# Kernel optimization log

Hardware: AMD Instinct MI355X
Metric: run time of the kernel (lower is better)

## Reference

```python
import jax, jax.numpy as jnp
import numpy as np

B, L, LF = 4096, 200, 100
E, P, H = 64, 32, 32      # embed_dim, prompt_embed_dim, prompt_net_hidden_size
IV, UV = 100000, 50000    # item/user vocab
IFD, UFD = 128, 128       # item/user raw feature dims
PNET = E * H + H + H * P + P  # per-sample MLP param count


def _forward(item_emb, user_emb, W_if, b_if, W_uf, b_uf, Wp, bp,
             Wf1, bf1, Wf2, bf2, Wf3, item_features, user_features,
             user_id, target_item_id, history_item_id, history_len,
             item_pos_feedback, item_pos_feedback_mask,
             item_neg_feedback, item_neg_feedback_mask):
    # ---- backbone embeddings ----
    tgt = item_emb[target_item_id]              # [B,E]
    hist = item_emb[history_item_id]            # [B,L,E]
    item_feat_e = jax.nn.sigmoid(item_features @ W_if + b_if)   # [B,E]
    user_feat_e = jax.nn.sigmoid(user_features @ W_uf + b_uf)   # [B,E]
    # attention sequence pooling over history (length-masked softmax)
    valid = jnp.arange(L)[None, :] < history_len[:, None]        # [B,L]
    scores = jnp.einsum('be,ble->bl', tgt, hist) / jnp.sqrt(jnp.float32(E))
    scores = jnp.where(valid, scores, jnp.float32(-1e9))
    attn = jax.nn.softmax(scores, axis=-1)
    hist_pooled = jnp.einsum('bl,ble->be', attn, hist)           # [B,E]
    final_user_embed = user_emb[user_id] + user_feat_e + hist_pooled  # [B,E]
    final_item_embed = tgt + item_feat_e                              # [B,E]

    # ---- prompt input: masked mean over positive feedback ----
    pos_fb = item_emb[item_pos_feedback]        # [B,LF,E]
    pm = item_pos_feedback_mask.astype(jnp.float32)   # [B,LF,1]
    prompt_input = (pos_fb * pm).sum(axis=1) / pm.sum(axis=1)   # [B,E]

    # ---- hypernetwork: generate per-sample MLP weights ----
    total_prompt = jax.nn.relu(prompt_input @ Wp + bp)  # [B, P+PNET]
    prompt_embed = total_prompt[:, :P]
    pnet = total_prompt[:, P:]
    s1 = E * H
    w1 = pnet[:, :s1].reshape(-1, E, H)                 # [B,E,H]
    b1 = pnet[:, s1:s1 + H]                             # [B,H]
    w2 = pnet[:, s1 + H:s1 + H + H * P].reshape(-1, H, P)  # [B,H,P]
    b2 = pnet[:, s1 + H + H * P:]                       # [B,P]

    def prompt_mlp(u):  # u: [B,Lf,E] -> [B,Lf,P]
        h = jax.nn.relu(jnp.einsum('ble,beh->blh', u, w1) + b1[:, None, :])
        return jnp.einsum('blh,bhp->blp', h, w2) + b2[:, None, :]

    pos_pe = jnp.where(item_pos_feedback_mask, prompt_mlp(pos_fb), 0.0).sum(axis=1)  # [B,P]
    neg_fb = item_emb[item_neg_feedback]
    neg_pe = jnp.where(item_neg_feedback_mask, prompt_mlp(neg_fb), 0.0).sum(axis=1)  # [B,P]
    loss_pfpe = jax.nn.softplus(-(pos_pe - neg_pe))     # [B,P]

    # ---- fusion + dot-product scoring ----
    fusion_in = jnp.concatenate([final_item_embed, pos_pe, prompt_embed], axis=1)  # [B,E+2P]
    h = jax.nn.relu(fusion_in @ Wf1 + bf1)
    h = jax.nn.relu(h @ Wf2 + bf2)
    fused_item = h @ Wf3                                # [B,E], last layer: no bias/act
    output = jnp.sum(final_user_embed * fused_item, axis=1, keepdims=True)  # [B,1]
    return output, loss_pfpe


def setup_inputs() -> dict:
    key = jax.random.key(0)
    ks = jax.random.split(key, 20)
    g = lambda i, shape, s=0.05: jax.random.normal(ks[i], shape, jnp.float32) * s
    pm = jax.random.randint(ks[14], (B, LF, 1), 0, 2).astype(bool).at[:, 0, :].set(True)
    nm = jax.random.randint(ks[15], (B, LF, 1), 0, 2).astype(bool).at[:, 0, :].set(True)
    return {
        'item_emb': g(0, (IV, E)),
        'user_emb': g(1, (UV, E)),
        'W_if': g(2, (IFD, E)), 'b_if': jnp.zeros((E,), jnp.float32),
        'W_uf': g(3, (UFD, E)), 'b_uf': jnp.zeros((E,), jnp.float32),
        'Wp': g(4, (E, P + PNET)), 'bp': jnp.zeros((P + PNET,), jnp.float32),
        'Wf1': g(5, (E + 2 * P, 200)), 'bf1': jnp.zeros((200,), jnp.float32),
        'Wf2': g(6, (200, 80)), 'bf2': jnp.zeros((80,), jnp.float32),
        'Wf3': g(7, (80, E)),
        'item_features': jax.random.normal(ks[8], (B, IFD), jnp.float32),
        'user_features': jax.random.normal(ks[9], (B, UFD), jnp.float32),
        'user_id': jax.random.randint(ks[10], (B,), 0, UV),
        'target_item_id': jax.random.randint(ks[11], (B,), 0, IV),
        'history_item_id': jax.random.randint(ks[12], (B, L), 0, IV),
        'history_len': jax.random.randint(ks[13], (B,), 1, L + 1),
        'item_pos_feedback': jax.random.randint(ks[16], (B, LF), 0, IV),
        'item_pos_feedback_mask': pm,
        'item_neg_feedback': jax.random.randint(ks[17], (B, LF), 0, IV),
        'item_neg_feedback_mask': nm,
    }


def reference(item_emb, user_emb, W_if, b_if, W_uf, b_uf, Wp, bp,
              Wf1, bf1, Wf2, bf2, Wf3, item_features, user_features,
              user_id, target_item_id, history_item_id, history_len,
              item_pos_feedback, item_pos_feedback_mask,
              item_neg_feedback, item_neg_feedback_mask):
    return _forward(item_emb, user_emb, W_if, b_if, W_uf, b_uf, Wp, bp,
                    Wf1, bf1, Wf2, bf2, Wf3, item_features, user_features,
                    user_id, target_item_id, history_item_id, history_len,
                    item_pos_feedback, item_pos_feedback_mask,
                    item_neg_feedback, item_neg_feedback_mask)
```

## Files before the change

### kernel.cpp

```cpp
#include <hip/hip_runtime.h>
#include <hip/hip_bf16.h>
#include <hip/hip_fp16.h>
#include <math.h>

#define BN 4096
#define LH 200
#define LFB 100
#define ED 64
#define PD 32
#define HD 32
#define NP 3168
#define IV 100000

typedef unsigned int uint32;
typedef __attribute__((ext_vector_type(8))) short short8;
typedef __attribute__((ext_vector_type(8))) _Float16 half8;
typedef __attribute__((ext_vector_type(4))) float f32x4;
union BF8 { uint32 u[4]; short8 v; };
union HF8 { uint32 u[4]; half8 v; };

__device__ __forceinline__ uint32 f2bf_pack(float x, float y) {
    uint32 ux = __float_as_uint(x);
    uint32 uy = __float_as_uint(y);
    uint32 bx = (ux + 0x7fffu + ((ux >> 16) & 1u)) >> 16;
    uint32 by = (uy + 0x7fffu + ((uy >> 16) & 1u)) >> 16;
    return (by << 16) | (bx & 0xffffu);
}

__device__ __forceinline__ uint32 f2h_pack(float x, float y) {
    __half2 h = __floats2half2_rn(x, y);
    return *(reinterpret_cast<uint32*>(&h));
}

__global__ __launch_bounds__(256) void k0_cvt(
    const float* __restrict__ src, uint32* __restrict__ dst)
{
    const int i = blockIdx.x * 256 + threadIdx.x;
    const float2 v = ((const float2*)src)[i];
    dst[i] = f2bf_pack(v.x, v.y);
}

__global__ __launch_bounds__(256) void k0b_cvt_wp(
    const float* __restrict__ Wp, uint32* __restrict__ WpB)
{
    const int n = blockIdx.x * 256 + threadIdx.x;
    const int kw = blockIdx.y;
    if (n < NP) {
        const float a = Wp[(size_t)(2*kw)*NP + n];
        const float b = Wp[(size_t)(2*kw+1)*NP + n];
        WpB[(size_t)n*32 + kw] = f2bf_pack(a, b);
    }
}

__global__ __launch_bounds__(256) void k0c_cvt_wf(
    const float* __restrict__ Wf1, const float* __restrict__ Wf2,
    const float* __restrict__ Wf3, uint32* __restrict__ W1B,
    uint32* __restrict__ W2B, uint32* __restrict__ W3B)
{
    const int i = blockIdx.x * 256 + threadIdx.x;
    if (i < 13312) {
        const int n = i >> 6, kw = i & 63;
        W1B[i] = (n < 200) ? f2h_pack(Wf1[(size_t)(2*kw)*200 + n],
                                      Wf1[(size_t)(2*kw+1)*200 + n]) : 0u;
    } else if (i < 22272) {
        const int j = i - 13312, n = j / 112, kw = j % 112;
        W2B[j] = (kw < 100) ? f2h_pack(Wf2[(size_t)(2*kw)*80 + n],
                                       Wf2[(size_t)(2*kw+1)*80 + n]) : 0u;
    } else if (i < 25344) {
        const int j = i - 22272, n = j / 48, kw = j % 48;
        W3B[j] = (kw < 40) ? f2h_pack(Wf3[(size_t)(2*kw)*64 + n],
                                      Wf3[(size_t)(2*kw+1)*64 + n]) : 0u;
    }
}

__global__ __launch_bounds__(256, 8) void k1_gather_attn(
    const uint32* __restrict__ IEB,
    const float* __restrict__ item_emb, const float* __restrict__ user_emb,
    const float* __restrict__ W_if, const float* __restrict__ b_if,
    const float* __restrict__ W_uf, const float* __restrict__ b_uf,
    const float* __restrict__ item_features, const float* __restrict__ user_features,
    const int* __restrict__ user_id, const int* __restrict__ target_item_id,
    const int* __restrict__ hist_id, const int* __restrict__ hist_len,
    const int* __restrict__ pos_fb, const int* __restrict__ pos_mask,
    float* __restrict__ FUE, float* __restrict__ FIE, uint32* __restrict__ PINB)
{
    const int b = blockIdx.x;
    const int t = threadIdx.x;
    const int w = t >> 6;
    const int lane = t & 63;

    __shared__ __align__(16) float tgt[64];
    __shared__ float feats[256];
    __shared__ float ufe[64];
    __shared__ float scoreS[256];
    __shared__ float wred[8];
    __shared__ float part[256];
    __shared__ float part2[256];
    __shared__ int   hids[200];
    __shared__ int   cpi[104];
    __shared__ int   ptot[2];

    const int hl = hist_len[b];
    if (t < 200) hids[t] = hist_id[(size_t)b*LH + t];
    feats[t] = (t < 128) ? item_features[(size_t)b*128 + t]
                         : user_features[(size_t)b*128 + (t-128)];
    if (t < 64) tgt[t] = item_emb[(size_t)target_item_id[b]*64 + t];

    bool myAct = false; int myPid = 0;
    if (t < LFB) {
        myAct = pos_mask[(size_t)b*LFB + t] != 0;
        myPid = pos_fb[(size_t)b*LFB + t];
    }
    __syncthreads();

    float sc = -1e9f;
    if (t < hl) {
        const uint4* rp = (const uint4*)(IEB + (size_t)hids[t]*32);
        float acc = 0.f;
        #pragma unroll
        for (int c4 = 0; c4 < 8; c4++) {
            const uint4 u = rp[c4];
            const uint32 ws[4] = {u.x, u.y, u.z, u.w};
            #pragma unroll
            for (int j = 0; j < 4; j++) {
                const float2 tf = ((const float2*)tgt)[c4*4 + j];
                acc = fmaf(__uint_as_float(ws[j] << 16),         tf.x, acc);
                acc = fmaf(__uint_as_float(ws[j] & 0xffff0000u), tf.y, acc);
            }
        }
        sc = acc * 0.125f;
    }

    int pre = 0;
    if (w < 2) {
        const unsigned long long bal = __ballot(myAct);
        pre = __popcll(bal & ((1ull << lane) - 1ull));
        if (lane == 0) ptot[w] = __popcll(bal);
    }

    float m = sc;
    #pragma unroll
    for (int off = 32; off >= 1; off >>= 1) m = fmaxf(m, __shfl_xor(m, off, 64));
    if (lane == 0) wred[w] = m;
    __syncthreads();

    const int nP = ptot[0] + ptot[1];
    if (w < 2 && myAct) cpi[((w == 1) ? ptot[0] : 0) + pre] = myPid;

    const float mx = fmaxf(fmaxf(wred[0], wred[1]), fmaxf(wred[2], wred[3]));
    const float ev = __expf(sc - mx);
    float s = ev;
    #pragma unroll
    for (int off = 32; off >= 1; off >>= 1) s += __shfl_xor(s, off, 64);
    if (lane == 0) wred[4 + w] = s;

    if (w == 0) {
        float acc = b_if[lane];
        #pragma unroll 4
        for (int k = 0; k < 128; k++) acc = fmaf(feats[k], W_if[k*64 + lane], acc);
        FIE[(size_t)b*64 + lane] = tgt[lane] + 1.f / (1.f + __expf(-acc));
    } else if (w == 1) {
        float acc = b_uf[lane];
        #pragma unroll 4
        for (int k = 0; k < 128; k++) acc = fmaf(feats[128 + k], W_uf[k*64 + lane], acc);
        ufe[lane] = 1.f / (1.f + __expf(-acc));
    }
    __syncthreads();

    const float S = wred[4] + wred[5] + wred[6] + wred[7];
    if (t < 200) scoreS[t] = ev / S;

    const int wk = lane >> 1;
    const int comp = lane & 1;
    {
        float pacc = 0.f;
        for (int i = w; i < nP; i += 4) {
            const uint32 wd = IEB[(size_t)cpi[i]*32 + wk];
            pacc += __uint_as_float(comp ? (wd & 0xffff0000u) : (wd << 16));
        }
        part2[w*64 + lane] = pacc;
    }
    __syncthreads();

    {
        float acc = 0.f;
        for (int l = w; l < hl; l += 4) {
            const uint32 word = IEB[(size_t)hids[l]*32 + wk];
            const float hv = __uint_as_float(comp ? (word & 0xffff0000u) : (word << 16));
            acc = fmaf(scoreS[l], hv, acc);
        }
        part[w*64 + lane] = acc;
    }
    __syncthreads();

    if (t < 64) {
        const float pooled = part[t] + part[64+t] + part[128+t] + part[192+t];
        const float pinv = (part2[t] + part2[64+t] + part2[128+t] + part2[192+t]) / (float)nP;
        FUE[(size_t)b*64 + t] = user_emb[(size_t)user_id[b]*64 + t] + ufe[t] + pooled;
        const float po = __shfl_xor(pinv, 1, 64);
        if ((t & 1) == 0) PINB[(size_t)b*32 + (t >> 1)] = f2bf_pack(pinv, po);
    }
}

__global__ __launch_bounds__(256) void k2_prompt_gemm(
    const uint32* __restrict__ PINB, const uint32* __restrict__ WpB,
    const float* __restrict__ bp, float* __restrict__ TP32,
    uint32* __restrict__ TPN)
{
    __shared__ uint32 As[64*36];
    __shared__ uint32 Bs[128*36];
    __shared__ float bps[128];
    const int t = threadIdx.x;
    const int m0 = blockIdx.y * 64;
    const int n0 = blockIdx.x * 128;

    {
        const int m = t >> 2, kw0 = (t & 3) * 8;
        const uint4 u0 = *(const uint4*)&PINB[(size_t)(m0+m)*32 + kw0];
        const uint4 u1 = *(const uint4*)&PINB[(size_t)(m0+m)*32 + kw0 + 4];
        *(uint4*)&As[m*36 + kw0]     = u0;
        *(uint4*)&As[m*36 + kw0 + 4] = u1;
    }
    {
        const int n = t >> 1, kw0 = (t & 1) * 16;
        const int gn = n0 + n;
        if (gn < NP) {
            #pragma unroll
            for (int j = 0; j < 4; j++) {
                const uint4 u = *(const uint4*)&WpB[(size_t)gn*32 + kw0 + 4*j];
                *(uint4*)&Bs[n*36 + kw0 + 4*j] = u;
            }
        } else {
            #pragma unroll
            for (int j = 0; j < 16; j++) Bs[n*36 + kw0 + j] = 0u;
        }
    }
    if (t < 128) bps[t] = (n0 + t < NP) ? bp[n0 + t] : 0.f;
    __syncthreads();

    const int w = t >> 6, lane = t & 63, ml = lane & 15, q = lane >> 4;

    BF8 a0, a1;
    { uint4 u = *(const uint4*)&As[(w*16+ml)*36 + q*4];      a0.u[0]=u.x; a0.u[1]=u.y; a0.u[2]=u.z; a0.u[3]=u.w; }
    { uint4 u = *(const uint4*)&As[(w*16+ml)*36 + 16 + q*4]; a1.u[0]=u.x; a1.u[1]=u.y; a1.u[2]=u.z; a1.u[3]=u.w; }

    f32x4 c[8];
    #pragma unroll
    for (int nb = 0; nb < 8; nb++) {
        BF8 b0, b1;
        { uint4 u = *(const uint4*)&Bs[(nb*16+ml)*36 + q*4];      b0.u[0]=u.x; b0.u[1]=u.y; b0.u[2]=u.z; b0.u[3]=u.w; }
        { uint4 u = *(const uint4*)&Bs[(nb*16+ml)*36 + 16 + q*4]; b1.u[0]=u.x; b1.u[1]=u.y; b1.u[2]=u.z; b1.u[3]=u.w; }
        f32x4 cc = {0.f, 0.f, 0.f, 0.f};
        cc = __builtin_amdgcn_mfma_f32_16x16x32_bf16(a0.v, b0.v, cc, 0, 0, 0);
        cc = __builtin_amdgcn_mfma_f32_16x16x32_bf16(a1.v, b1.v, cc, 0, 0, 0);
        c[nb] = cc;
    }

    #pragma unroll
    for (int nb = 0; nb < 8; nb++) {
        const int n = n0 + nb*16 + ml;
        const float bv = bps[nb*16 + ml];
        #pragma unroll
        for (int r = 0; r < 4; r++) {
            const int m = m0 + w*16 + q*4 + r;
            const float v = fmaxf(c[nb][r] + bv, 0.f);
            const float vp = __shfl_xor(v, 1, 64);
            if (n < 32) {
                TP32[(size_t)m*32 + n] = v;
            } else if (n < NP && (ml & 1) == 0) {
                TPN[(size_t)m*1568 + ((n - 32) >> 1)] = f2bf_pack(v, vp);
            }
        }
    }
}

__global__ __launch_bounds__(256) void k3_prompt_mlp(
    const uint32* __restrict__ IEB,
    const int* __restrict__ pos_fb, const int* __restrict__ pos_mask,
    const int* __restrict__ neg_fb, const int* __restrict__ neg_mask,
    const uint32* __restrict__ TPN,
    float* __restrict__ POS_PE, float* __restrict__ out)
{
    const int b = blockIdx.x, t = threadIdx.x;
    const int w = t >> 6, lane = t & 63;
    const int ml = lane & 15, q = lane >> 4;

    __shared__ uint32 w1b[32*36];
    __shared__ uint32 w2b[32*20];
    __shared__ float b1s[32], b2s[32];
    __shared__ float mPs[208], mNs[208];
    __shared__ int cids[208];
    __shared__ int tot[4];
    __shared__ float Hs[4][16*36];
    __shared__ float wps[4][4][16];

    bool act = false; int id = 0;
    if (t < LFB) {
        act = pos_mask[(size_t)b*LFB + t] != 0;
        id  = pos_fb[(size_t)b*LFB + t];
    } else if (t >= 128 && t < 128 + LFB) {
        act = neg_mask[(size_t)b*LFB + (t-128)] != 0;
        id  = neg_fb[(size_t)b*LFB + (t-128)];
    }
    const unsigned long long bal = __ballot(act);
    const int pre = __popcll(bal & ((1ull << lane) - 1ull));
    if (lane == 0) tot[w] = __popcll(bal);
    if (t < 208) cids[t] = 0;

    const uint32* pnw = TPN + (size_t)b*1568;
    #pragma unroll
    for (int it = 0; it < 4; it++) {
        const int i = t + 256*it;
        const int n = i >> 5, kw = i & 31;
        const uint32 wa = pnw[kw*32 + (n >> 1)];
        const uint32 wb = pnw[kw*32 + 16 + (n >> 1)];
        const uint32 h0 = (n & 1) ? (wa >> 16) : (wa & 0xffffu);
        const uint32 h1 = (n & 1) ? (wb >> 16) : (wb & 0xffffu);
        w1b[n*36 + kw] = h0 | (h1 << 16);
    }
    #pragma unroll
    for (int it = 0; it < 2; it++) {
        const int i = t + 256*it;
        const int n = i >> 4, kw = i & 15;
        const uint32 wa = pnw[1040 + kw*32 + (n >> 1)];
        const uint32 wb = pnw[1040 + kw*32 + 16 + (n >> 1)];
        const uint32 h0 = (n & 1) ? (wa >> 16) : (wa & 0xffffu);
        const uint32 h1 = (n & 1) ? (wb >> 16) : (wb & 0xffffu);
        w2b[n*20 + kw] = h0 | (h1 << 16);
    }
    if (t < 16) {
        const uint32 wa = pnw[1024 + t];
        b1s[2*t]   = __uint_as_float(wa << 16);
        b1s[2*t+1] = __uint_as_float(wa & 0xffff0000u);
        const uint32 wb = pnw[1552 + t];
        b2s[2*t]   = __uint_as_float(wb << 16);
        b2s[2*t+1] = __uint_as_float(wb & 0xffff0000u);
    }
    __syncthreads();

    const int nP = tot[0] + tot[1];
    const int nN = tot[2] + tot[3];
    const int R  = nP + nN;
    const int T  = (R + 15) >> 4;
    {
        int base = 0;
        if (w == 1) base = tot[0];
        else if (w == 2) base = nP;
        else if (w == 3) base = nP + tot[2];
        if (act) cids[base + pre] = id;
    }
    if (t < 208) {
        mPs[t] = (t < nP) ? 1.f : 0.f;
        mNs[t] = (t >= nP && t < R) ? 1.f : 0.f;
    }

    BF8 bf100, bf110, bf101, bf111, bf20, bf21;
    {
        uint4 u;
        u = *(const uint4*)&w1b[ml*36 + q*4];            bf100.u[0]=u.x; bf100.u[1]=u.y; bf100.u[2]=u.z; bf100.u[3]=u.w;
        u = *(const uint4*)&w1b[ml*36 + 16 + q*4];       bf110.u[0]=u.x; bf110.u[1]=u.y; bf110.u[2]=u.z; bf110.u[3]=u.w;
        u = *(const uint4*)&w1b[(16+ml)*36 + q*4];       bf101.u[0]=u.x; bf101.u[1]=u.y; bf101.u[2]=u.z; bf101.u[3]=u.w;
        u = *(const uint4*)&w1b[(16+ml)*36 + 16 + q*4];  bf111.u[0]=u.x; bf111.u[1]=u.y; bf111.u[2]=u.z; bf111.u[3]=u.w;
        u = *(const uint4*)&w2b[ml*20 + q*4];            bf20.u[0]=u.x;  bf20.u[1]=u.y;  bf20.u[2]=u.z;  bf20.u[3]=u.w;
        u = *(const uint4*)&w2b[(16+ml)*20 + q*4];       bf21.u[0]=u.x;  bf21.u[1]=u.y;  bf21.u[2]=u.z;  bf21.u[3]=u.w;
    }
    __syncthreads();

    float accP0=0.f, accP1=0.f, accN0=0.f, accN1=0.f;
    float* hsw = Hs[w];

    for (int tile = w; tile < T; tile += 4) {
        const int g = tile*16 + ml;
        const uint32* rowp = IEB + (size_t)cids[g]*32;
        BF8 a0, a1;
        { uint4 u = *(const uint4*)(rowp + q*4);      a0.u[0]=u.x; a0.u[1]=u.y; a0.u[2]=u.z; a0.u[3]=u.w; }
        { uint4 u = *(const uint4*)(rowp + 16 + q*4); a1.u[0]=u.x; a1.u[1]=u.y; a1.u[2]=u.z; a1.u[3]=u.w; }

        f32x4 c0 = {0.f,0.f,0.f,0.f}, c1 = {0.f,0.f,0.f,0.f};
        c0 = __builtin_amdgcn_mfma_f32_16x16x32_bf16(a0.v, bf100.v, c0, 0, 0, 0);
        c0 = __builtin_amdgcn_mfma_f32_16x16x32_bf16(a1.v, bf110.v, c0, 0, 0, 0);
        c1 = __builtin_amdgcn_mfma_f32_16x16x32_bf16(a0.v, bf101.v, c1, 0, 0, 0);
        c1 = __builtin_amdgcn_mfma_f32_16x16x32_bf16(a1.v, bf111.v, c1, 0, 0, 0);

        #pragma unroll
        for (int r = 0; r < 4; r++) {
            const int row = q*4 + r;
            hsw[row*36 + ml]      = fmaxf(c0[r] + b1s[ml],      0.f);
            hsw[row*36 + 16 + ml] = fmaxf(c1[r] + b1s[16 + ml], 0.f);
        }
        asm volatile("s_waitcnt lgkmcnt(0)" ::: "memory");

        const float4 h0 = *(const float4*)&hsw[ml*36 + q*8];
        const float4 h1 = *(const float4*)&hsw[ml*36 + q*8 + 4];
        BF8 a2;
        a2.u[0] = f2bf_pack(h0.x, h0.y);
        a2.u[1] = f2bf_pack(h0.z, h0.w);
        a2.u[2] = f2bf_pack(h1.x, h1.y);
        a2.u[3] = f2bf_pack(h1.z, h1.w);

        f32x4 d0 = {0.f,0.f,0.f,0.f}, d1 = {0.f,0.f,0.f,0.f};
        d0 = __builtin_amdgcn_mfma_f32_16x16x32_bf16(a2.v, bf20.v, d0, 0, 0, 0);
        d1 = __builtin_amdgcn_mfma_f32_16x16x32_bf16(a2.v, bf21.v, d1, 0, 0, 0);

        #pragma unroll
        for (int r = 0; r < 4; r++) {
            const int g2 = tile*16 + q*4 + r;
            const float o0 = d0[r] + b2s[ml];
            const float o1 = d1[r] + b2s[16 + ml];
            accP0 = fmaf(mPs[g2], o0, accP0);
            accP1 = fmaf(mPs[g2], o1, accP1);
            accN0 = fmaf(mNs[g2], o0, accN0);
            accN1 = fmaf(mNs[g2], o1, accN1);
        }
    }

    accP0 += __shfl_xor(accP0, 16, 64); accP0 += __shfl_xor(accP0, 32, 64);
    accP1 += __shfl_xor(accP1, 16, 64); accP1 += __shfl_xor(accP1, 32, 64);
    accN0 += __shfl_xor(accN0, 16, 64); accN0 += __shfl_xor(accN0, 32, 64);
    accN1 += __shfl_xor(accN1, 16, 64); accN1 += __shfl_xor(accN1, 32, 64);
    if (lane < 16) {
        wps[w][0][lane] = accP0;
        wps[w][1][lane] = accP1;
        wps[w][2][lane] = accN0;
        wps[w][3][lane] = accN1;
    }
    __syncthreads();

    if (t < 32) {
        const int nt = t >> 4, p = t & 15;
        const float pp = wps[0][nt][p] + wps[1][nt][p] + wps[2][nt][p] + wps[3][nt][p];
        const float nn = wps[0][2+nt][p] + wps[1][2+nt][p] + wps[2][2+nt][p] + wps[3][2+nt][p];
        POS_PE[(size_t)b*32 + t] = pp;
        const float x = nn - pp;
        out[BN + (size_t)b*32 + t] = fmaxf(x, 0.f) + log1pf(__expf(-fabsf(x)));
    }
}

__global__ __launch_bounds__(256) void k4_fusion(
    const float* __restrict__ FUE, const float* __restrict__ FIE,
    const float* __restrict__ POS_PE, const float* __restrict__ TP32,
    const uint32* __restrict__ W1B, const uint32* __restrict__ W2B,
    const uint32* __restrict__ W3B,
    const float* __restrict__ bf1, const float* __restrict__ bf2,
    float* __restrict__ out)
{
    const int b0 = blockIdx.x * 16;
    const int t = threadIdx.x;
    const int w = t >> 6, lane = t & 63, ml = lane & 15, q = lane >> 4;

    __shared__ uint32 w1s[208*68];
    __shared__ uint32 w2s[80*116];
    __shared__ uint32 w3s[64*52];
    __shared__ uint32 fin[16*68];
    __shared__ uint32 h1w[16*116];
    __shared__ uint32 h2w[16*52];
    __shared__ float fuels[16*68];
    __shared__ float b1s[208], b2s[80];
    __shared__ float part4[4][16];

    for (int i = t; i < 13312; i += 256) w1s[(i >> 6)*68 + (i & 63)] = W1B[i];
    for (int i = t; i < 8960; i += 256)  w2s[(i / 112)*116 + (i % 112)] = W2B[i];
    for (int i = t; i < 3072; i += 256)  w3s[(i / 48)*52 + (i % 48)] = W3B[i];

    #pragma unroll
    for (int it = 0; it < 4; it++) {
        const int i = t + 256*it;
        const int m2 = i >> 6, kw = i & 63;
        const int row = b0 + m2;
        float a, c;
        if (kw < 32)      { const float2 v = *(const float2*)&FIE[(size_t)row*64 + 2*kw];          a = v.x; c = v.y; }
        else if (kw < 48) { const float2 v = *(const float2*)&POS_PE[(size_t)row*32 + 2*kw - 64];  a = v.x; c = v.y; }
        else              { const float2 v = *(const float2*)&TP32[(size_t)row*32 + 2*kw - 96];    a = v.x; c = v.y; }
        fin[m2*68 + kw] = f2h_pack(a, c);
        fuels[m2*68 + kw] = FUE[(size_t)row*64 + kw];
    }
    if (t < 208) b1s[t] = (t < 200) ? bf1[t] : 0.f;
    if (t < 80)  b2s[t] = bf2[t];
    if (t < 128) {
        h1w[(t >> 3)*116 + 104 + (t & 7)] = 0u;
        h2w[(t >> 3)*52 + 40 + (t & 7)] = 0u;
    }
    __syncthreads();

    HF8 a1f[4];
    #pragma unroll
    for (int s = 0; s < 4; s++) {
        const uint4 u = *(const uint4*)&fin[ml*68 + s*16 + q*4];
        a1f[s].u[0] = u.x; a1f[s].u[1] = u.y; a1f[s].u[2] = u.z; a1f[s].u[3] = u.w;
    }
    for (int nt = w; nt < 13; nt += 4) {
        const uint32* wrow = &w1s[(16*nt + ml)*68];
        f32x4 c = {0.f, 0.f, 0.f, 0.f};
        #pragma unroll
        for (int s = 0; s < 4; s++) {
            HF8 bfm;
            const uint4 u = *(const uint4*)&wrow[s*16 + q*4];
            bfm.u[0] = u.x; bfm.u[1] = u.y; bfm.u[2] = u.z; bfm.u[3] = u.w;
            c = __builtin_amdgcn_mfma_f32_16x16x32_f16(a1f[s].v, bfm.v, c, 0, 0, 0);
        }
        const float bv = b1s[16*nt + ml];
        #pragma unroll
        for (int r = 0; r < 4; r++) {
            const float v = fmaxf(c[r] + bv, 0.f);
            const float vp = __shfl_xor(v, 1, 64);
            if ((ml & 1) == 0)
                h1w[(q*4 + r)*116 + 8*nt + (ml >> 1)] = f2h_pack(v, vp);
        }
    }
    __syncthreads();

    HF8 a2f[7];
    #pragma unroll
    for (int s = 0; s < 7; s++) {
        const uint4 u = *(const uint4*)&h1w[ml*116 + s*16 + q*4];
        a2f[s].u[0] = u.x; a2f[s].u[1] = u.y; a2f[s].u[2] = u.z; a2f[s].u[3] = u.w;
    }
    for (int nt = w; nt < 5; nt += 4) {
        const uint32* wrow = &w2s[(16*nt + ml)*116];
        f32x4 c = {0.f, 0.f, 0.f, 0.f};
        #pragma unroll
        for (int s = 0; s < 7; s++) {
            HF8 bfm;
            const uint4 u = *(const uint4*)&wrow[s*16 + q*4];
            bfm.u[0] = u.x; bfm.u[1] = u.y; bfm.u[2] = u.z; bfm.u[3] = u.w;
            c = __builtin_amdgcn_mfma_f32_16x16x32_f16(a2f[s].v, bfm.v, c, 0, 0, 0);
        }
        const float bv = b2s[16*nt + ml];
        #pragma unroll
        for (int r = 0; r < 4; r++) {
            const float v = fmaxf(c[r] + bv, 0.f);
            const float vp = __shfl_xor(v, 1, 64);
            if ((ml & 1) == 0)
                h2w[(q*4 + r)*52 + 8*nt + (ml >> 1)] = f2h_pack(v, vp);
        }
    }
    __syncthreads();

    {
        const int nt = w;
        const uint32* wrow = &w3s[(16*nt + ml)*52];
        f32x4 c = {0.f, 0.f, 0.f, 0.f};
        #pragma unroll
        for (int s = 0; s < 3; s++) {
            HF8 afm, bfm;
            const uint4 ua = *(const uint4*)&h2w[ml*52 + s*16 + q*4];
            afm.u[0] = ua.x; afm.u[1] = ua.y; afm.u[2] = ua.z; afm.u[3] = ua.w;
            const uint4 ub = *(const uint4*)&wrow[s*16 + q*4];
            bfm.u[0] = ub.x; bfm.u[1] = ub.y; bfm.u[2] = ub.z; bfm.u[3] = ub.w;
            c = __builtin_amdgcn_mfma_f32_16x16x32_f16(afm.v, bfm.v, c, 0, 0, 0);
        }
        #pragma unroll
        for (int r = 0; r < 4; r++) {
            float p = c[r] * fuels[(q*4 + r)*68 + 16*nt + ml];
            p += __shfl_xor(p, 1, 64);
            p += __shfl_xor(p, 2, 64);
            p += __shfl_xor(p, 4, 64);
            p += __shfl_xor(p, 8, 64);
            if (ml == 0) part4[w][q*4 + r] = p;
        }
    }
    __syncthreads();

    if (t < 16) out[b0 + t] = part4[0][t] + part4[1][t] + part4[2][t] + part4[3][t];
}

extern "C" void kernel_launch(void* const* d_in, const int* in_sizes, int n_in,
                              void* d_out, int out_size, void* d_ws, size_t ws_size,
                              hipStream_t stream)
{
    const float* item_emb       = (const float*)d_in[0];
    const float* user_emb       = (const float*)d_in[1];
    const float* W_if           = (const float*)d_in[2];
    const float* b_if           = (const float*)d_in[3];
    const float* W_uf           = (const float*)d_in[4];
    const float* b_uf           = (const float*)d_in[5];
    const float* Wp             = (const float*)d_in[6];
    const float* bp             = (const float*)d_in[7];
    const float* Wf1            = (const float*)d_in[8];
    const float* bf1            = (const float*)d_in[9];
    const float* Wf2            = (const float*)d_in[10];
    const float* bf2            = (const float*)d_in[11];
    const float* Wf3            = (const float*)d_in[12];
    const float* item_features  = (const float*)d_in[13];
    const float* user_features  = (const float*)d_in[14];
    const int*   user_id        = (const int*)d_in[15];
    const int*   target_item_id = (const int*)d_in[16];
    const int*   history_item_id= (const int*)d_in[17];
    const int*   history_len    = (const int*)d_in[18];
    const int*   pos_fb         = (const int*)d_in[19];
    const int*   pos_mask       = (const int*)d_in[20];
    const int*   neg_fb         = (const int*)d_in[21];
    const int*   neg_mask       = (const int*)d_in[22];

    float* out = (float*)d_out;
    float* ws  = (float*)d_ws;

    uint32* IEB  = (uint32*)ws;
    uint32* WpB  = IEB + (size_t)IV*32;
    uint32* W1B  = WpB + (size_t)NP*32;
    uint32* W2B  = W1B + 13312;
    uint32* W3B  = W2B + 8960;
    uint32* PINB = W3B + 3072;
    float*  FUE  = (float*)(PINB + (size_t)BN*32);
    float*  FIE  = FUE + (size_t)BN*64;
    float*  TP32 = FIE + (size_t)BN*64;
    uint32* TPN  = (uint32*)(TP32 + (size_t)BN*32);
    float*  PPE  = (float*)(TPN + (size_t)BN*1568);

    k0_cvt<<<dim3(IV*32/256), dim3(256), 0, stream>>>(item_emb, IEB);
    k0b_cvt_wp<<<dim3(13, 32), dim3(256), 0, stream>>>(Wp, WpB);
    k0c_cvt_wf<<<dim3(99), dim3(256), 0, stream>>>(Wf1, Wf2, Wf3, W1B, W2B, W3B);

    k1_gather_attn<<<dim3(BN), dim3(256), 0, stream>>>(
        IEB, item_emb, user_emb, W_if, b_if, W_uf, b_uf,
        item_features, user_features, user_id, target_item_id,
        history_item_id, history_len, pos_fb, pos_mask,
        FUE, FIE, PINB);

    k2_prompt_gemm<<<dim3(25, 64), dim3(256), 0, stream>>>(PINB, WpB, bp, TP32, TPN);

    k3_prompt_mlp<<<dim3(BN), dim3(256), 0, stream>>>(
        IEB, pos_fb, pos_mask, neg_fb, neg_mask, TPN, PPE, out);

    k4_fusion<<<dim3(BN/16), dim3(256), 0, stream>>>(
        FUE, FIE, PPE, TP32, W1B, W2B, W3B, bf1, bf2, out);
}
```

Measured before the change: 280.5 us.

## Load history rows once into registers for scores and pooling; transpose k3 weight staging

In the gather/attention kernel, each history row is now fetched once with coalesced 32-lane loads and held in registers. The attention scores come from shuffle reductions, and the same registers are reused for the weighted pooling instead of a second gather from the embedding table. The positive-feedback mean is moved earlier to overlap with the softmax work, and the occupancy hint drops from 8 to 6 blocks per CU to make room for the 25-register row buffer. In the prompt MLP kernel, the per-sample weight staging in shared memory is transposed so that global reads and shared-memory writes are contiguous, in exchange for scalar rather than vector shared loads when forming the MFMA B fragments.

```diff
diff --git a/kernel.cpp b/kernel.cpp
--- a/kernel.cpp
+++ b/kernel.cpp
@@ -73,7 +73,7 @@
     }
 }
 
-__global__ __launch_bounds__(256, 8) void k1_gather_attn(
+__global__ __launch_bounds__(256, 6) void k1_gather_attn(
     const uint32* __restrict__ IEB,
     const float* __restrict__ item_emb, const float* __restrict__ user_emb,
     const float* __restrict__ W_if, const float* __restrict__ b_if,
@@ -113,22 +113,28 @@
     }
     __syncthreads();
 
-    float sc = -1e9f;
-    if (t < hl) {
-        const uint4* rp = (const uint4*)(IEB + (size_t)hids[t]*32);
-        float acc = 0.f;
-        #pragma unroll
-        for (int c4 = 0; c4 < 8; c4++) {
-            const uint4 u = rp[c4];
-            const uint32 ws[4] = {u.x, u.y, u.z, u.w};
-            #pragma unroll
-            for (int j = 0; j < 4; j++) {
-                const float2 tf = ((const float2*)tgt)[c4*4 + j];
-                acc = fmaf(__uint_as_float(ws[j] << 16),         tf.x, acc);
-                acc = fmaf(__uint_as_float(ws[j] & 0xffff0000u), tf.y, acc);
-            }
-        }
-        sc = acc * 0.125f;
+    const int kk = lane & 31;
+    const int hf = lane >> 5;
+    const float2 tf = ((const float2*)tgt)[kk];
+
+    uint32 rw[25];
+    #pragma unroll
+    for (int i = 0; i < 25; i++) {
+        const int l = w*50 + i*2 + hf;
+        rw[i] = (l < hl) ? IEB[(size_t)hids[l]*32 + kk] : 0u;
+    }
+
+    #pragma unroll
+    for (int i = 0; i < 25; i++) {
+        const int l = w*50 + i*2 + hf;
+        float sp = fmaf(__uint_as_float(rw[i] << 16), tf.x,
+                        __uint_as_float(rw[i] & 0xffff0000u) * tf.y);
+        sp += __shfl_xor(sp, 1, 64);
+        sp += __shfl_xor(sp, 2, 64);
+        sp += __shfl_xor(sp, 4, 64);
+        sp += __shfl_xor(sp, 8, 64);
+        sp += __shfl_xor(sp, 16, 64);
+        if (kk == 0) scoreS[l] = sp * 0.125f;
     }
 
     int pre = 0;
@@ -137,15 +143,17 @@
         pre = __popcll(bal & ((1ull << lane) - 1ull));
         if (lane == 0) ptot[w] = __popcll(bal);
     }
-
+    __syncthreads();
+
+    const int nP = ptot[0] + ptot[1];
+    if (w < 2 && myAct) cpi[((w == 1) ? ptot[0] : 0) + pre] = myPid;
+
+    float sc = (t < hl) ? scoreS[t] : -1e9f;
     float m = sc;
     #pragma unroll
     for (int off = 32; off >= 1; off >>= 1) m = fmaxf(m, __shfl_xor(m, off, 64));
     if (lane == 0) wred[w] = m;
     __syncthreads();
-
-    const int nP = ptot[0] + ptot[1];
-    if (w < 2 && myAct) cpi[((w == 1) ? ptot[0] : 0) + pre] = myPid;
 
     const float mx = fmaxf(fmaxf(wred[0], wred[1]), fmaxf(wred[2], wred[3]));
     const float ev = __expf(sc - mx);
@@ -153,6 +161,17 @@
     #pragma unroll
     for (int off = 32; off >= 1; off >>= 1) s += __shfl_xor(s, off, 64);
     if (lane == 0) wred[4 + w] = s;
+
+    const int wk = lane >> 1;
+    const int comp = lane & 1;
+    {
+        float pacc = 0.f;
+        for (int i = w; i < nP; i += 4) {
+            const uint32 wd = IEB[(size_t)cpi[i]*32 + wk];
+            pacc += __uint_as_float(comp ? (wd & 0xffff0000u) : (wd << 16));
+        }
+        part2[w*64 + lane] = pacc;
+    }
 
     if (w == 0) {
         float acc = b_if[lane];
@@ -169,27 +188,23 @@
 
     const float S = wred[4] + wred[5] + wred[6] + wred[7];
     if (t < 200) scoreS[t] = ev / S;
-
-    const int wk = lane >> 1;
-    const int comp = lane & 1;
+    __syncthreads();
+
     {
-        float pacc = 0.f;
-        for (int i = w; i < nP; i += 4) {
-            const uint32 wd = IEB[(size_t)cpi[i]*32 + wk];
-            pacc += __uint_as_float(comp ? (wd & 0xffff0000u) : (wd << 16));
-        }
-        part2[w*64 + lane] = pacc;
-    }
-    __syncthreads();
-
-    {
-        float acc = 0.f;
-        for (int l = w; l < hl; l += 4) {
-            const uint32 word = IEB[(size_t)hids[l]*32 + wk];
-            const float hv = __uint_as_float(comp ? (word & 0xffff0000u) : (word << 16));
-            acc = fmaf(scoreS[l], hv, acc);
-        }
-        part[w*64 + lane] = acc;
+        float ax = 0.f, ay = 0.f;
+        #pragma unroll
+        for (int i = 0; i < 25; i++) {
+            const int l = w*50 + i*2 + hf;
+            const float a = scoreS[l];
+            ax = fmaf(a, __uint_as_float(rw[i] << 16),         ax);
+            ay = fmaf(a, __uint_as_float(rw[i] & 0xffff0000u), ay);
+        }
+        ax += __shfl_xor(ax, 32, 64);
+        ay += __shfl_xor(ay, 32, 64);
+        if (hf == 0) {
+            part[w*64 + 2*kk]     = ax;
+            part[w*64 + 2*kk + 1] = ay;
+        }
     }
     __syncthreads();
 
@@ -285,8 +300,8 @@
     const int w = t >> 6, lane = t & 63;
     const int ml = lane & 15, q = lane >> 4;
 
-    __shared__ uint32 w1b[32*36];
-    __shared__ uint32 w2b[32*20];
+    __shared__ uint32 w1T[32*36];
+    __shared__ uint32 w2T[16*36];
     __shared__ float b1s[32], b2s[32];
     __shared__ float mPs[208], mNs[208];
     __shared__ int cids[208];
@@ -311,22 +326,22 @@
     #pragma unroll
     for (int it = 0; it < 4; it++) {
         const int i = t + 256*it;
-        const int n = i >> 5, kw = i & 31;
+        const int kw = i >> 5, n = i & 31;
         const uint32 wa = pnw[kw*32 + (n >> 1)];
         const uint32 wb = pnw[kw*32 + 16 + (n >> 1)];
         const uint32 h0 = (n & 1) ? (wa >> 16) : (wa & 0xffffu);
         const uint32 h1 = (n & 1) ? (wb >> 16) : (wb & 0xffffu);
-        w1b[n*36 + kw] = h0 | (h1 << 16);
+        w1T[kw*36 + n] = h0 | (h1 << 16);
     }
     #pragma unroll
     for (int it = 0; it < 2; it++) {
         const int i = t + 256*it;
-        const int n = i >> 4, kw = i & 15;
+        const int kw = i >> 5, n = i & 31;
         const uint32 wa = pnw[1040 + kw*32 + (n >> 1)];
         const uint32 wb = pnw[1040 + kw*32 + 16 + (n >> 1)];
         const uint32 h0 = (n & 1) ? (wa >> 16) : (wa & 0xffffu);
         const uint32 h1 = (n & 1) ? (wb >> 16) : (wb & 0xffffu);
-        w2b[n*20 + kw] = h0 | (h1 << 16);
+        w2T[kw*36 + n] = h0 | (h1 << 16);
     }
     if (t < 16) {
         const uint32 wa = pnw[1024 + t];
@@ -355,14 +370,14 @@
     }
 
     BF8 bf100, bf110, bf101, bf111, bf20, bf21;
-    {
-        uint4 u;
-        u = *(const uint4*)&w1b[ml*36 + q*4];            bf100.u[0]=u.x; bf100.u[1]=u.y; bf100.u[2]=u.z; bf100.u[3]=u.w;
-        u = *(const uint4*)&w1b[ml*36 + 16 + q*4];       bf110.u[0]=u.x; bf110.u[1]=u.y; bf110.u[2]=u.z; bf110.u[3]=u.w;
-        u = *(const uint4*)&w1b[(16+ml)*36 + q*4];       bf101.u[0]=u.x; bf101.u[1]=u.y; bf101.u[2]=u.z; bf101.u[3]=u.w;
-        u = *(const uint4*)&w1b[(16+ml)*36 + 16 + q*4];  bf111.u[0]=u.x; bf111.u[1]=u.y; bf111.u[2]=u.z; bf111.u[3]=u.w;
-        u = *(const uint4*)&w2b[ml*20 + q*4];            bf20.u[0]=u.x;  bf20.u[1]=u.y;  bf20.u[2]=u.z;  bf20.u[3]=u.w;
-        u = *(const uint4*)&w2b[(16+ml)*20 + q*4];       bf21.u[0]=u.x;  bf21.u[1]=u.y;  bf21.u[2]=u.z;  bf21.u[3]=u.w;
+    #pragma unroll
+    for (int j = 0; j < 4; j++) {
+        bf100.u[j] = w1T[(q*4+j)*36 + ml];
+        bf110.u[j] = w1T[(16+q*4+j)*36 + ml];
+        bf101.u[j] = w1T[(q*4+j)*36 + 16 + ml];
+        bf111.u[j] = w1T[(16+q*4+j)*36 + 16 + ml];
+        bf20.u[j]  = w2T[(q*4+j)*36 + ml];
+        bf21.u[j]  = w2T[(q*4+j)*36 + 16 + ml];
     }
     __syncthreads();
 
```

Measured after the change: 237.9 us. 15.2% less time.
